# Kernel tuning notes

Measured on AMD Instinct MI355X. Metric: run time of the kernel, lower is better.

Reference implementation:

```python
import jax, jax.numpy as jnp
import numpy as np

# WFN symmetry table: symmetry index -> (px, py, pz) angular-momentum exponents
# (s; px,py,pz; 6 cartesian d; 10 cartesian f) as in standard .wfn files.
WFN_SYMMETRY_INDEX = np.array([
    [0, 0, 0],
    [1, 0, 0], [0, 1, 0], [0, 0, 1],
    [2, 0, 0], [0, 2, 0], [0, 0, 2], [1, 1, 0], [1, 0, 1], [0, 1, 1],
    [3, 0, 0], [0, 3, 0], [0, 0, 3], [2, 1, 0], [2, 0, 1], [0, 2, 1],
    [1, 2, 0], [1, 0, 2], [0, 1, 2], [1, 1, 1],
], dtype=np.float32)


def setup_inputs() -> dict:
    key = jax.random.key(0)
    k1, k2, k3, k4, k5 = jax.random.split(key, 5)
    n, ms, na, nps = 16, 4096, 32, 512
    dv = jax.random.normal(k1, (n, ms, na, 3), jnp.float32)          # sample->atom displacement vectors
    centers = jax.random.randint(k2, (n, nps), 0, na)                # primitive -> atom index (-1 = pad)
    exp = jax.random.uniform(k3, (n, nps), jnp.float32)              # GTO exponents (>0)
    sym = jax.random.randint(k4, (n, nps), 0, 20)                    # symmetry index into WFN table
    dm = jax.random.normal(k5, (n, nps, nps), jnp.float32) / nps     # density matrices
    return {"dv": dv, "centers": centers, "exp": exp, "sym": sym, "dm": dm}


def _density(dv, exp, dm, centers, sym):
    # dv: [n,ms,na,3]; exp: [n,np]; dm: [n,np,np]; centers/sym: [n,np] int
    sym_map = jnp.asarray(WFN_SYMMETRY_INDEX)
    valid = centers >= 0                                   # padded primitives marked -1
    c = jnp.where(valid, centers, 0)
    s = jnp.where(valid, sym, 0)
    r2 = jnp.sum(dv * dv, axis=-1)                         # [n,ms,na] squared distances
    r2g = jax.vmap(lambda r, ci: r[:, ci])(r2, c)          # [n,ms,np] gather per primitive
    dvg = jax.vmap(lambda d, ci: d[:, ci])(dv, c)          # [n,ms,np,3]
    pw = sym_map[s]                                        # [n,np,3] angular exponents
    # GTO kernel: dx^px * dy^py * dz^pz * exp(-alpha * r^2)
    ang = jnp.prod(jnp.power(dvg, pw[:, None, :, :]), axis=-1)   # [n,ms,np]
    basis = ang * jnp.exp(-exp[:, None, :] * r2g)
    basis = basis * valid[:, None, :].astype(basis.dtype)        # zero out padded primitives
    # rho = sum_pq basis_p * dm_pq * basis_q (per molecule, per sample point)
    return jnp.einsum('nmp,npq,nmq->nm', basis, dm, basis)


def reference(dv, centers, exp, sym, dm):
    return _density(dv, exp, dm, centers, sym)
```

## Files before the change

### kernel.cpp

```cpp
#include <hip/hip_runtime.h>
#include <stdint.h>

#define NMOL 16
#define MS   4096
#define NA   32
#define NP   512
#define BM   64
#define TBL  65536u

typedef __attribute__((ext_vector_type(4))) float  f32x4;
typedef __attribute__((ext_vector_type(4))) unsigned int u32x4;
typedef __attribute__((ext_vector_type(2))) unsigned int u32x2;
typedef __attribute__((ext_vector_type(8))) short  s16x8;
typedef unsigned int uint;
typedef unsigned short ushort;

#define WS_DMF_OFF   0u
#define WS_DMF_SZ    (16u*512u*512u*2u)
#define WS_M2A_OFF   (WS_DMF_OFF + WS_DMF_SZ)
#define WS_M2A_SZ    (16u*512u*4u)
#define WS_M2B_OFF   (WS_M2A_OFF + WS_M2A_SZ)
#define WS_M2B_SZ    (16u*512u*4u)
#define WS_ALPH_OFF  (WS_M2B_OFF + WS_M2B_SZ)

__device__ __constant__ uint c_pw[20] = {
  0x000,
  0x001, 0x010, 0x100,
  0x002, 0x020, 0x200, 0x011, 0x101, 0x110,
  0x003, 0x030, 0x300, 0x012, 0x102, 0x120, 0x021, 0x201, 0x210, 0x111
};

__device__ __forceinline__ ushort f2bf(float f) {
  uint u = __float_as_uint(f);
  u = u + 0x7fffu + ((u >> 16) & 1u);
  return (ushort)(u >> 16);
}
__device__ __forceinline__ float bflo(uint u) { return __uint_as_float(u << 16); }
__device__ __forceinline__ float bfhi(uint u) { return __uint_as_float(u & 0xFFFF0000u); }
__device__ __forceinline__ float cvt16lo(uint u) {
  float r; asm("v_cvt_f32_f16 %0, %1" : "=v"(r) : "v"(u)); return r;
}
__device__ __forceinline__ float cvt16hi(uint u) {
  uint s = u >> 16; float r; asm("v_cvt_f32_f16 %0, %1" : "=v"(r) : "v"(s)); return r;
}
__device__ __forceinline__ uint pkmul(uint a, uint b) {
  uint r; asm("v_pk_mul_f16 %0, %1, %2" : "=v"(r) : "v"(a), "v"(b)); return r;
}
__device__ __forceinline__ s16x8 mkfrag(u32x2 lo, u32x2 hi) {
  union { uint u[4]; s16x8 v; } x;
  x.u[0] = lo[0]; x.u[1] = lo[1]; x.u[2] = hi[0]; x.u[3] = hi[1];
  return x.v;
}

__global__ void dm_pack(const float* __restrict__ dm, short* __restrict__ dmF,
                        const int* __restrict__ centers, const int* __restrict__ sym,
                        const float* __restrict__ expg,
                        uint* __restrict__ m2a, uint* __restrict__ m2b,
                        float* __restrict__ alphaS) {
  __shared__ float tile[NP * 33];
  const int Qp = blockIdx.x, n = blockIdx.y;
  const int t = threadIdx.x;
  const float* base = dm + (size_t)n * NP * NP;
  const float* src  = base + Qp * 32;
#pragma unroll
  for (int i = 0; i < 64; ++i) {
    int e = t + 256 * i;
    int p = e >> 5, c = e & 31;
    tile[p * 33 + c] = src[(size_t)p * NP + c];
  }
  if (n == 0) {
#pragma unroll
    for (int kk = 0; kk < 2; ++kk) {
      int i = Qp * 512 + t + 256 * kk;
      int craw = centers[i], s = sym[i];
      bool valid = (craw >= 0);
      uint c = (uint)((valid ? craw : 0) & (NA - 1));
      int si = valid ? s : 0;
      si = (si >= 0 && si < 20) ? si : 0;
      uint pw = c_pw[si];
      uint d = (pw & 15u) + ((pw >> 4) & 15u) + ((pw >> 8) & 15u);
      uint h[3]; int k = 0;
#pragma unroll
      for (uint ax = 0; ax < 3; ++ax) {
        uint e2 = (pw >> (4 * ax)) & 15u;
        for (uint r = 0; r < e2; ++r) if (k < 3) h[k++] = c * 512u + ax * 128u;
      }
      while (k < 3) h[k++] = c * 512u;
      m2a[i] = h[0] | (h[1] << 16);
      m2b[i] = h[2] | (d << 14) | (c << 16);
      alphaS[i] = (valid ? -expg[i] : -1e5f) * 1.44269504088896f;
    }
  }
  __syncthreads();
#pragma unroll
  for (int it = 0; it < 8; ++it) {
    int v = t + 256 * it;
    int qq = v >> 10, vv = v & 1023;
    int kblk = vv >> 6, l = vv & 63;
    int p0 = kblk * 32 + ((l >> 4) << 3);
    int col = l & 15;
    int q = (Qp * 2 + qq) * 16 + col;
    f32x4 r0 = *(const f32x4*)(base + (size_t)q * NP + p0);
    f32x4 r1 = *(const f32x4*)(base + (size_t)q * NP + p0 + 4);
    s16x8 o;
#pragma unroll
    for (int j = 0; j < 8; ++j) {
      int p = p0 + j;
      float tpq = tile[p * 33 + qq * 16 + col];
      float rv = (j < 4) ? r0[j] : r1[j - 4];
      float w = (p < q) ? (tpq + rv) : ((p == q) ? tpq : 0.0f);
      o[j] = (short)f2bf(w);
    }
    short* dst = dmF + ((size_t)(n * 32 + Qp * 2 + qq) * 16) * 512;
    *(s16x8*)(dst + (size_t)vv * 8) = o;
  }
}

__device__ __forceinline__ void basis_slice(char* smem, uint ma, uint mb, float al,
                                            int p, int jb) {
  uint h0 = ma & 0xFFFFu, h1 = ma >> 16, h2 = mb & 0x3FFFu;
  uint d  = (mb >> 14) & 3u;
  uint cs = (h0 >> 9) & 7u;
  uint rh = (h0 & 0xFE00u) + 384u;
  const bool ge2 = (d >= 2), eq3 = (d == 3), eq0 = (d == 0);
  uint wbase = (((uint)p >> 5) << 10) + ((((uint)p >> 2) & 1u) << 9)
             + ((((uint)p & 31u) >> 3) << 7) + (((uint)p & 3u) << 5);
#pragma unroll
  for (int jo = 0; jo < 2; ++jo) {
    int j = jb + jo;
    uint off = (uint)((j ^ (int)cs) << 4);
    u32x4 qr = *(const u32x4*)(smem + TBL + rh + off);
    u32x4 q0, q1, q2;
    if (!eq0) q0 = *(const u32x4*)(smem + TBL + h0 + off);
    if (ge2)  q1 = *(const u32x4*)(smem + TBL + h1 + off);
    if (eq3)  q2 = *(const u32x4*)(smem + TBL + h2 + off);
    uint res[4];
#pragma unroll
    for (int w = 0; w < 4; ++w) {
      uint m_ = eq0 ? 0x3C003C00u : q0[w];
      if (ge2) m_ = pkmul(m_, q1[w]);
      if (eq3) m_ = pkmul(m_, q2[w]);
      float r2l = cvt16lo(qr[w]), r2h = cvt16hi(qr[w]);
      float a0 = al * r2l, a1 = al * r2h;
      float e0, e1;
      asm("v_exp_f32 %0, %1" : "=v"(e0) : "v"(a0));
      asm("v_exp_f32 %0, %1" : "=v"(e1) : "v"(a1));
      float v0 = cvt16lo(m_) * e0, v1 = cvt16hi(m_) * e1;
      asm("v_cvt_pk_bf16_f32 %0, %1, %2" : "=v"(res[w]) : "v"(v0), "v"(v1));
    }
    *(u32x4*)(smem + wbase + ((uint)(j >> 1) << 14) + ((uint)(j & 1) << 4)) = *(u32x4*)res;
  }
}

#define MFMA16(a, b, c) __builtin_amdgcn_mfma_f32_16x16x32_bf16(a, b, c, 0, 0, 0)

#define ISSUE_TR(AK) \
  asm volatile("ds_read_b64_tr_b16 %0, %1 offset:0"     : "=v"(l0) : "v"(AK)); \
  asm volatile("ds_read_b64_tr_b16 %0, %1 offset:512"   : "=v"(g0) : "v"(AK)); \
  asm volatile("ds_read_b64_tr_b16 %0, %1 offset:16384" : "=v"(l1) : "v"(AK)); \
  asm volatile("ds_read_b64_tr_b16 %0, %1 offset:16896" : "=v"(g1) : "v"(AK)); \
  asm volatile("ds_read_b64_tr_b16 %0, %1 offset:32768" : "=v"(l2) : "v"(AK)); \
  asm volatile("ds_read_b64_tr_b16 %0, %1 offset:33280" : "=v"(g2) : "v"(AK)); \
  asm volatile("ds_read_b64_tr_b16 %0, %1 offset:49152" : "=v"(l3) : "v"(AK)); \
  asm volatile("ds_read_b64_tr_b16 %0, %1 offset:49664" : "=v"(g3) : "v"(AK));

#define FINISH_TRIP(KBLK) do { \
  s16x8 bf0, bf1, bf2, bf3; \
  const bool c0 = (KBLK) <= kq0, c1 = (KBLK) <= kq1, c2 = (KBLK) <= kq2; \
  if (c0) bf0 = *(const s16x8*)(bp0 + (KBLK) * 512); \
  if (c1) bf1 = *(const s16x8*)(bp1 + (KBLK) * 512); \
  if (c2) bf2 = *(const s16x8*)(bp2 + (KBLK) * 512); \
  bf3 = *(const s16x8*)(bp3 + (KBLK) * 512); \
  asm volatile("s_waitcnt lgkmcnt(0)"); \
  __builtin_amdgcn_sched_barrier(0); \
  s16x8 af0 = mkfrag(l0, g0), af1 = mkfrag(l1, g1); \
  s16x8 af2 = mkfrag(l2, g2), af3 = mkfrag(l3, g3); \
  __builtin_amdgcn_s_setprio(1); \
  if (c0) { acc[0][0]=MFMA16(af0,bf0,acc[0][0]); acc[1][0]=MFMA16(af1,bf0,acc[1][0]); \
            acc[2][0]=MFMA16(af2,bf0,acc[2][0]); acc[3][0]=MFMA16(af3,bf0,acc[3][0]); } \
  if (c1) { acc[0][1]=MFMA16(af0,bf1,acc[0][1]); acc[1][1]=MFMA16(af1,bf1,acc[1][1]); \
            acc[2][1]=MFMA16(af2,bf1,acc[2][1]); acc[3][1]=MFMA16(af3,bf1,acc[3][1]); } \
  if (c2) { acc[0][2]=MFMA16(af0,bf2,acc[0][2]); acc[1][2]=MFMA16(af1,bf2,acc[1][2]); \
            acc[2][2]=MFMA16(af2,bf2,acc[2][2]); acc[3][2]=MFMA16(af3,bf2,acc[3][2]); } \
  acc[0][3]=MFMA16(af0,bf3,acc[0][3]); acc[1][3]=MFMA16(af1,bf3,acc[1][3]); \
  acc[2][3]=MFMA16(af2,bf3,acc[2][3]); acc[3][3]=MFMA16(af3,bf3,acc[3][3]); \
  __builtin_amdgcn_s_setprio(0); \
} while (0)

__launch_bounds__(512, 4)
__global__ void wfn_fused8(const float* __restrict__ dv,
                           const uint* __restrict__ m2aG,
                           const uint* __restrict__ m2bG,
                           const float* __restrict__ alG,
                           const short* __restrict__ dmF,
                           float* __restrict__ out) {
  __shared__ __align__(16) char smem[81920];
  const int t = threadIdx.x;
  const int bid = ((blockIdx.x & 7) << 7) + (blockIdx.x >> 3);
  const int n  = bid >> 6;
  const int m0 = (bid & 63) * BM;

  {
    const float* dvg = dv + (size_t)(n * MS + m0) * (NA * 3);
#pragma unroll
    for (int k = 0; k < 4; ++k) {
      int idx = t + 512 * k;
      int m = idx >> 5, c = idx & 31;
      const float* p = dvg + (m * NA + c) * 3;
      float x = p[0], y = p[1], z = p[2];
      float r2 = fmaf(x, x, fmaf(y, y, z * z));
      uint base = TBL + (uint)c * 512u
                + ((uint)((m >> 3) ^ (c & 7)) << 4) + (uint)((m & 7) << 1);
      *(_Float16*)(smem + base)       = (_Float16)x;
      *(_Float16*)(smem + base + 128) = (_Float16)y;
      *(_Float16*)(smem + base + 256) = (_Float16)z;
      *(_Float16*)(smem + base + 384) = (_Float16)r2;
    }
  }
  __syncthreads();

  const int pl = t & 127;
  const int jb = (t >> 7) * 2;
  const int mbase = n * NP;
  uint cma, cmb; float cal;
  {
    cma = m2aG[mbase + 128 + pl]; cmb = m2bG[mbase + 128 + pl]; cal = alG[mbase + 128 + pl];
    uint a0 = m2aG[mbase + pl];  uint b0 = m2bG[mbase + pl];  float l0_ = alG[mbase + pl];
    basis_slice(smem, a0, b0, l0_, pl, jb);
  }
  __syncthreads();

  const int lane = t & 63, wv = t >> 6, li = lane & 15, kg = lane >> 4;
  const uint lane8 = (uint)lane << 3;
  const short* dmFn = dmF + (size_t)n * (32 * 16 * 512);

  f32x4 acc[4][4];
#pragma unroll
  for (int rf = 0; rf < 4; ++rf)
#pragma unroll
    for (int qf = 0; qf < 4; ++qf)
      acc[rf][qf] = (f32x4){0.f, 0.f, 0.f, 0.f};

  const short* bp0 = dmFn + ((size_t)((wv)      * 16) * 512) + lane * 8;
  const short* bp1 = dmFn + ((size_t)((wv + 8)  * 16) * 512) + lane * 8;
  const short* bp2 = dmFn + ((size_t)((wv + 16) * 16) * 512) + lane * 8;
  const short* bp3 = dmFn + ((size_t)((wv + 24) * 16) * 512) + lane * 8;
  const int kq0 = wv >> 1, kq1 = (wv + 8) >> 1, kq2 = (wv + 16) >> 1;
  const int kmaxw = (wv + 24) >> 1;

  for (int cnk = 0; cnk < 4; ++cnk) {
    const int kbeg = cnk * 4;
    const int kend = (cnk < 3) ? (kbeg + 3) : kmaxw;
    {
      uint ak = lane8 + ((uint)kbeg << 10);
      u32x2 l0, g0, l1, g1, l2, g2, l3, g3;
      ISSUE_TR(ak);
      if (cnk < 3) {
        uint nma = 0u, nmb = 0u; float nal = 0.f;
        if (cnk < 2) {
          int mp = mbase + (cnk + 2) * 128 + pl;
          nma = m2aG[mp]; nmb = m2bG[mp]; nal = alG[mp];
        }
        basis_slice(smem, cma, cmb, cal, (cnk + 1) * 128 + pl, jb);
        cma = nma; cmb = nmb; cal = nal;
      }
      FINISH_TRIP(kbeg);
    }
    for (int kblk = kbeg + 1; kblk <= kend; ++kblk) {
      uint ak = lane8 + ((uint)kblk << 10);
      u32x2 l0, g0, l1, g1, l2, g2, l3, g3;
      ISSUE_TR(ak);
      FINISH_TRIP(kblk);
    }
    if (cnk < 3) __syncthreads();
  }

  float part[16];
#pragma unroll
  for (int x = 0; x < 16; ++x) part[x] = 0.0f;
  uint qp[4];
#pragma unroll
  for (int qf = 0; qf < 4; ++qf) {
    int q = (wv + 8 * qf) * 16 + li;
    qp[qf] = ((uint)(q >> 5) << 10) + (((uint)(q >> 2) & 1u) << 9)
           + (((uint)(q & 31) >> 3) << 7) + ((uint)(q & 3) << 5) + ((uint)kg << 3);
  }
#pragma unroll
  for (int rf = 0; rf < 4; ++rf) {
#pragma unroll
    for (int qf = 0; qf < 4; ++qf) {
      u32x2 dq = *(const u32x2*)(smem + ((uint)rf << 14) + qp[qf]);
      part[rf * 4 + 0] = fmaf(acc[rf][qf][0], bflo(dq[0]), part[rf * 4 + 0]);
      part[rf * 4 + 1] = fmaf(acc[rf][qf][1], bfhi(dq[0]), part[rf * 4 + 1]);
      part[rf * 4 + 2] = fmaf(acc[rf][qf][2], bflo(dq[1]), part[rf * 4 + 2]);
      part[rf * 4 + 3] = fmaf(acc[rf][qf][3], bfhi(dq[1]), part[rf * 4 + 3]);
    }
  }

  __syncthreads();
#pragma unroll
  for (int x = 0; x < 16; ++x) {
    float v = part[x];
    v += __shfl_xor(v, 1);
    v += __shfl_xor(v, 2);
    v += __shfl_xor(v, 4);
    v += __shfl_xor(v, 8);
    part[x] = v;
  }
  float* rbuf = (float*)smem;
  if (li == 0) {
#pragma unroll
    for (int rf = 0; rf < 4; ++rf)
#pragma unroll
      for (int jj = 0; jj < 4; ++jj)
        rbuf[wv * 64 + rf * 16 + kg * 4 + jj] = part[rf * 4 + jj];
  }
  __syncthreads();
  if (t < BM) {
    float s = 0.0f;
#pragma unroll
    for (int w = 0; w < 8; ++w) s += rbuf[w * 64 + t];
    out[(size_t)n * MS + m0 + t] = s;
  }
}

extern "C" void kernel_launch(void* const* d_in, const int* in_sizes, int n_in,
                              void* d_out, int out_size, void* d_ws, size_t ws_size,
                              hipStream_t stream) {
  const float* dv      = (const float*)d_in[0];
  const int*   centers = (const int*)d_in[1];
  const float* expg    = (const float*)d_in[2];
  const int*   sym     = (const int*)d_in[3];
  const float* dm      = (const float*)d_in[4];
  float* out = (float*)d_out;

  char* ws = (char*)d_ws;
  short* dmF    = (short*)(ws + WS_DMF_OFF);
  uint*  m2a    = (uint*)(ws + WS_M2A_OFF);
  uint*  m2b    = (uint*)(ws + WS_M2B_OFF);
  float* alphaS = (float*)(ws + WS_ALPH_OFF);

  dm_pack<<<dim3(16, NMOL), 256, 0, stream>>>(dm, dmF, centers, sym, expg,
                                              m2a, m2b, alphaS);
  wfn_fused8<<<dim3(NMOL * (MS / BM)), 512, 0, stream>>>(dv, m2a, m2b, alphaS, dmF, out);
}
```

Measured before the change: 57.41 us.

## Compute full basis tile upfront instead of interleaving chunks with MFMA loop

Removes the chunked software pipeline that computed the basis in 128-primitive slices interleaved with the MFMA k-loop and separated by barriers. Each thread now computes the basis for one primitive across all 8 sample groups before a single barrier, then runs one uninterrupted MFMA loop. This drops three intra-loop barriers and the staged prefetch logic, at the cost of no longer overlapping exp/basis work with matrix math.

```diff
diff --git a/kernel.cpp b/kernel.cpp
--- a/kernel.cpp
+++ b/kernel.cpp
@@ -113,42 +113,6 @@
     }
     short* dst = dmF + ((size_t)(n * 32 + Qp * 2 + qq) * 16) * 512;
     *(s16x8*)(dst + (size_t)vv * 8) = o;
-  }
-}
-
-__device__ __forceinline__ void basis_slice(char* smem, uint ma, uint mb, float al,
-                                            int p, int jb) {
-  uint h0 = ma & 0xFFFFu, h1 = ma >> 16, h2 = mb & 0x3FFFu;
-  uint d  = (mb >> 14) & 3u;
-  uint cs = (h0 >> 9) & 7u;
-  uint rh = (h0 & 0xFE00u) + 384u;
-  const bool ge2 = (d >= 2), eq3 = (d == 3), eq0 = (d == 0);
-  uint wbase = (((uint)p >> 5) << 10) + ((((uint)p >> 2) & 1u) << 9)
-             + ((((uint)p & 31u) >> 3) << 7) + (((uint)p & 3u) << 5);
-#pragma unroll
-  for (int jo = 0; jo < 2; ++jo) {
-    int j = jb + jo;
-    uint off = (uint)((j ^ (int)cs) << 4);
-    u32x4 qr = *(const u32x4*)(smem + TBL + rh + off);
-    u32x4 q0, q1, q2;
-    if (!eq0) q0 = *(const u32x4*)(smem + TBL + h0 + off);
-    if (ge2)  q1 = *(const u32x4*)(smem + TBL + h1 + off);
-    if (eq3)  q2 = *(const u32x4*)(smem + TBL + h2 + off);
-    uint res[4];
-#pragma unroll
-    for (int w = 0; w < 4; ++w) {
-      uint m_ = eq0 ? 0x3C003C00u : q0[w];
-      if (ge2) m_ = pkmul(m_, q1[w]);
-      if (eq3) m_ = pkmul(m_, q2[w]);
-      float r2l = cvt16lo(qr[w]), r2h = cvt16hi(qr[w]);
-      float a0 = al * r2l, a1 = al * r2h;
-      float e0, e1;
-      asm("v_exp_f32 %0, %1" : "=v"(e0) : "v"(a0));
-      asm("v_exp_f32 %0, %1" : "=v"(e1) : "v"(a1));
-      float v0 = cvt16lo(m_) * e0, v1 = cvt16hi(m_) * e1;
-      asm("v_cvt_pk_bf16_f32 %0, %1, %2" : "=v"(res[w]) : "v"(v0), "v"(v1));
-    }
-    *(u32x4*)(smem + wbase + ((uint)(j >> 1) << 14) + ((uint)(j & 1) << 4)) = *(u32x4*)res;
   }
 }
 
@@ -219,14 +183,43 @@
   }
   __syncthreads();
 
-  const int pl = t & 127;
-  const int jb = (t >> 7) * 2;
-  const int mbase = n * NP;
-  uint cma, cmb; float cal;
   {
-    cma = m2aG[mbase + 128 + pl]; cmb = m2bG[mbase + 128 + pl]; cal = alG[mbase + 128 + pl];
-    uint a0 = m2aG[mbase + pl];  uint b0 = m2bG[mbase + pl];  float l0_ = alG[mbase + pl];
-    basis_slice(smem, a0, b0, l0_, pl, jb);
+    const int p = t;
+    const uint ma = m2aG[n * NP + p], mb = m2bG[n * NP + p];
+    const float al = alG[n * NP + p];
+    const uint h0 = ma & 0xFFFFu, h1 = ma >> 16;
+    const uint h2 = mb & 0x3FFFu;
+    const uint d  = (mb >> 14) & 3u;
+    const uint cs = (h0 >> 9) & 7u;
+    const uint rh = (h0 & 0xFE00u) + 384u;
+    const bool ge2 = (d >= 2), eq3 = (d == 3), eq0 = (d == 0);
+    const uint wbase = ((uint)(p >> 5) << 10) + (((uint)(p >> 2) & 1u) << 9)
+                     + ((((uint)p & 31u) >> 3) << 7) + (((uint)p & 3u) << 5);
+#pragma unroll
+    for (int j = 0; j < 8; ++j) {
+      uint off = (uint)((j ^ (int)cs) << 4);
+      u32x4 qr = *(const u32x4*)(smem + TBL + rh + off);
+      u32x4 q0, q1, q2;
+      if (!eq0) q0 = *(const u32x4*)(smem + TBL + h0 + off);
+      if (ge2)  q1 = *(const u32x4*)(smem + TBL + h1 + off);
+      if (eq3)  q2 = *(const u32x4*)(smem + TBL + h2 + off);
+      uint res[4];
+#pragma unroll
+      for (int w = 0; w < 4; ++w) {
+        uint m_ = eq0 ? 0x3C003C00u : q0[w];
+        if (ge2) m_ = pkmul(m_, q1[w]);
+        if (eq3) m_ = pkmul(m_, q2[w]);
+        float r2l = cvt16lo(qr[w]), r2h = cvt16hi(qr[w]);
+        float a0 = al * r2l, a1 = al * r2h;
+        float e0, e1;
+        asm("v_exp_f32 %0, %1" : "=v"(e0) : "v"(a0));
+        asm("v_exp_f32 %0, %1" : "=v"(e1) : "v"(a1));
+        float v0 = cvt16lo(m_) * e0, v1 = cvt16hi(m_) * e1;
+        asm("v_cvt_pk_bf16_f32 %0, %1, %2" : "=v"(res[w]) : "v"(v0), "v"(v1));
+      }
+      *(u32x4*)(smem + wbase + ((uint)(j >> 1) << 14) + ((uint)(j & 1) << 4))
+          = *(u32x4*)res;
+    }
   }
   __syncthreads();
 
@@ -248,31 +241,11 @@
   const int kq0 = wv >> 1, kq1 = (wv + 8) >> 1, kq2 = (wv + 16) >> 1;
   const int kmaxw = (wv + 24) >> 1;
 
-  for (int cnk = 0; cnk < 4; ++cnk) {
-    const int kbeg = cnk * 4;
-    const int kend = (cnk < 3) ? (kbeg + 3) : kmaxw;
-    {
-      uint ak = lane8 + ((uint)kbeg << 10);
-      u32x2 l0, g0, l1, g1, l2, g2, l3, g3;
-      ISSUE_TR(ak);
-      if (cnk < 3) {
-        uint nma = 0u, nmb = 0u; float nal = 0.f;
-        if (cnk < 2) {
-          int mp = mbase + (cnk + 2) * 128 + pl;
-          nma = m2aG[mp]; nmb = m2bG[mp]; nal = alG[mp];
-        }
-        basis_slice(smem, cma, cmb, cal, (cnk + 1) * 128 + pl, jb);
-        cma = nma; cmb = nmb; cal = nal;
-      }
-      FINISH_TRIP(kbeg);
-    }
-    for (int kblk = kbeg + 1; kblk <= kend; ++kblk) {
-      uint ak = lane8 + ((uint)kblk << 10);
-      u32x2 l0, g0, l1, g1, l2, g2, l3, g3;
-      ISSUE_TR(ak);
-      FINISH_TRIP(kblk);
-    }
-    if (cnk < 3) __syncthreads();
+  for (int kblk = 0; kblk <= kmaxw; ++kblk) {
+    uint ak = lane8 + ((uint)kblk << 10);
+    u32x2 l0, g0, l1, g1, l2, g2, l3, g3;
+    ISSUE_TR(ak);
+    FINISH_TRIP(kblk);
   }
 
   float part[16];
```

Result: faster. 49.72 us (-13.4%).
